# Optimization experiments

Hardware: AMD Instinct MI355X
Metric: run time of the kernel (lower is better)

## Reference

```python
import jax
import jax.numpy as jnp
from jax import lax
import numpy as np

# module hyperparameters (match init_kwargs)
IN_C, OUT_C = 32, 64
K, STRIDE, PAD, DIL = 3, 1, 1, 1
GRID_SIZE, ORDER = 5, 3
GRID_LO, GRID_HI = -1.0, 1.0
SCALE_SPLINE = 1.0
EPS = 1e-8


def _knot_grid():
    # grid = arange(-order, grid_size+order+1) * h + lo ; length = grid_size + 2*order + 1 = 12
    h = (GRID_HI - GRID_LO) / GRID_SIZE
    return jnp.arange(-ORDER, GRID_SIZE + ORDER + 1, dtype=jnp.float32) * h + GRID_LO


def _bspline_bases(x):
    """Cox-de Boor recursion. x: (N, P) -> bases: (N, P, GRID_SIZE+ORDER)."""
    grid = _knot_grid()
    xe = x[..., None]  # (N, P, 1)
    bases = ((xe >= grid[:-1]) & (xe < grid[1:])).astype(x.dtype)  # (N, P, 11)
    for k in range(1, ORDER + 1):
        left_den = jnp.maximum(grid[k:-1] - grid[:-(k + 1)], EPS)
        right_den = jnp.maximum(grid[k + 1:] - grid[1:-k], EPS)
        bases = ((xe - grid[:-(k + 1)]) / left_den * bases[..., :-1]
                 + (grid[k + 1:] - xe) / right_den * bases[..., 1:])
    return bases  # (N, P, 8)


def setup_inputs() -> dict:
    key = jax.random.key(0)
    k1, k2, k3 = jax.random.split(key, 3)
    x = jax.random.normal(k1, (4, IN_C, 56, 56), dtype=jnp.float32)
    base_weight = jax.random.normal(k2, (OUT_C, IN_C, K, K), dtype=jnp.float32) * 0.05
    spline_weight = jax.random.normal(k3, (OUT_C, IN_C * K * K, GRID_SIZE + ORDER), dtype=jnp.float32) * 0.05
    spline_scaler = jnp.ones((OUT_C,), dtype=jnp.float32)
    return {"x": x, "base_weight": base_weight,
            "spline_weight": spline_weight, "spline_scaler": spline_scaler}


def reference(x, base_weight, spline_weight, spline_scaler):
    B, C, H, W = x.shape
    pad = [(PAD, PAD), (PAD, PAD)]
    # base path: conv2d -> SiLU
    base_conv = lax.conv_general_dilated(
        x, base_weight, window_strides=(STRIDE, STRIDE), padding=pad,
        rhs_dilation=(DIL, DIL), dimension_numbers=("NCHW", "OIHW", "NCHW"))
    base_out = jax.nn.silu(base_conv)

    # unfold: (B, C*K*K, oh, ow) with torch Unfold channel ordering (c, kh, kw)
    patches = lax.conv_general_dilated_patches(
        x, filter_shape=(K, K), window_strides=(STRIDE, STRIDE), padding=pad,
        rhs_dilation=(DIL, DIL))
    oh, ow = patches.shape[2], patches.shape[3]
    num_patches = oh * ow
    # (B*num_patches, C*K*K)
    pf = patches.reshape(B, C * K * K, num_patches).transpose(0, 2, 1).reshape(-1, C * K * K)

    bases = _bspline_bases(pf)  # (N, P, F)
    # contract patch-dim and basis-dim against spline weights
    spl = jnp.einsum("npf,opf->no", bases, spline_weight) * spline_scaler  # (N, O)
    spl = spl.reshape(B, num_patches, OUT_C).transpose(0, 2, 1).reshape(B, OUT_C, oh, ow)
    return base_out + SCALE_SPLINE * spl
```

## Files before the change

### kernel.cpp

```cpp
#include <hip/hip_runtime.h>
#include <math.h>


typedef __attribute__((ext_vector_type(8)))  short bf16x8;
typedef __attribute__((ext_vector_type(4)))  float f32x4;
typedef __attribute__((ext_vector_type(16))) float f32x16;

#define MFMA32(a, b, c) __builtin_amdgcn_mfma_f32_32x32x16_bf16((a), (b), (c), 0, 0, 0)

__device__ __forceinline__ unsigned short f2bf(float f) {
    unsigned u = __builtin_bit_cast(unsigned, f);
    u = (u + 0x7fffu + ((u >> 16) & 1u)) >> 16;
    return (unsigned short)u;
}

__device__ __forceinline__ void eval_bases(float v, float bs[8]) {
    #pragma unroll
    for (int i = 0; i < 8; ++i) bs[i] = 0.0f;
    float t = (v + 2.2f) * 2.5f;
    if (t >= 0.0f && t < 11.0f) {
        int j = (int)t;
        if (j > 10) j = 10;
        float knot = (float)(j - 3) * 0.4f - 1.0f;
        float u  = (v - knot) * 2.5f;
        float um = 1.0f - u;
        float u2 = u * u, u3 = u2 * u;
        const float s6 = 1.0f / 6.0f;
        float w0 = um * um * um * s6;
        float w1 = (3.0f * u3 - 6.0f * u2 + 4.0f) * s6;
        float w2 = (-3.0f * u3 + 3.0f * u2 + 3.0f * u + 1.0f) * s6;
        float w3 = u3 * s6;
        int i0 = j - 3;
        if (i0 >= 0)               bs[i0]     = w0;
        if (i0 + 1 >= 0 && i0 < 7) bs[i0 + 1] = w1;
        if (i0 + 2 >= 0 && i0 < 6) bs[i0 + 2] = w2;
        if (i0 + 3 <= 7)           bs[i0 + 3] = w3;
    }
}

__global__ __launch_bounds__(256)
void cvt_swz_kernel(const float* __restrict__ ws, const float* __restrict__ wb,
                    unsigned short* __restrict__ wst, unsigned short* __restrict__ wbt) {
    int i = blockIdx.x * 256 + threadIdx.x;
    if (i < 147456) {
        int j = i & 7, l = (i >> 3) & 63, t = i >> 9;
        int s = t % 144, nf = t / 144;
        int oc = nf * 32 + (l & 31);
        int k  = s * 16 + (l >> 5) * 8 + j;
        wst[i] = f2bf(ws[oc * 2304 + k]);
    } else {
        int i2 = i - 147456;
        if (i2 < 18432) {
            int j = i2 & 7, l = (i2 >> 3) & 63, t = i2 >> 9;
            int s = t % 18, nf = t / 18;
            int oc = nf * 32 + (l & 31);
            int k  = s * 16 + (l >> 5) * 8 + j;
            wbt[i2] = f2bf(wb[oc * 288 + k]);
        }
    }
}

__global__ __launch_bounds__(256, 3)
void kan_mfma_kernel(const float* __restrict__ x,
                     const float* __restrict__ sc,
                     const unsigned short* __restrict__ wst,
                     const unsigned short* __restrict__ wbt,
                     float* __restrict__ out) {
    __shared__ unsigned short smem[24832];
    unsigned short* sb    = smem;
    unsigned short* patch = smem + 15360;

    const int tid = threadIdx.x;
    const int bx  = blockIdx.x;
    const int b   = bx / 98;
    const int r   = bx - b * 98;
    const int ty  = r / 7;
    const int tx  = r - ty * 7;
    const int h0  = ty * 4, w0 = tx * 8;

    const int lane = tid & 63;
    const int wv   = tid >> 6;
    const int nf   = wv & 1;
    const int kh2  = wv >> 1;
    const int m    = lane & 31;
    const int kg   = lane >> 5;
    const int py0  = m >> 3, px0 = m & 7;

    const unsigned short* bp  = wst + ((nf * 144 + kh2 * 72) * 64 + lane) * 8;
    const unsigned short* bbp = wbt + ((nf * 18  + kh2 * 9 ) * 64 + lane) * 8;

    int aoff[9];
    #pragma unroll
    for (int u = 0; u < 9; ++u) {
        int t2  = 2 * u + kg;
        int dc  = t2 / 9;
        int tap = t2 - dc * 9;
        int kh  = tap / 3;
        int kw  = tap - kh * 3;
        aoff[u] = (dc * 60 + (py0 + kh) * 10 + (px0 + kw)) * 8;
    }

    bf16x8 bufA[9], bufB[9];
    #pragma unroll
    for (int u = 0; u < 9; ++u)
        bufA[u] = *reinterpret_cast<const bf16x8*>(bp + u * 512);

    float vv[8];
    #pragma unroll
    for (int j = 0; j < 8; ++j) {
        int i = tid + j * 256;
        float val = 0.0f;
        if (i < 1920) {
            int c  = i / 60;
            int hp = i - c * 60;
            int hy = hp / 10;
            int hx = hp - hy * 10;
            int hh = h0 + hy - 1, ww = w0 + hx - 1;
            if ((unsigned)hh < 56u && (unsigned)ww < 56u)
                val = x[((b * 32 + c) * 56 + hh) * 56 + ww];
        }
        vv[j] = val;
    }
    #pragma unroll
    for (int j = 0; j < 8; ++j) {
        int i = tid + j * 256;
        if (i < 1920) {
            int c  = i / 60;
            int hp = i - c * 60;
            int hy = hp / 10;
            int hx = hp - hy * 10;
            float bs[8];
            eval_bases(vv[j], bs);
            bf16x8 pk;
            #pragma unroll
            for (int j2 = 0; j2 < 8; ++j2) pk[j2] = (short)f2bf(bs[j2]);
            *reinterpret_cast<bf16x8*>(&sb[i * 8]) = pk;
            unsigned short xb = f2bf(vv[j]);
            #pragma unroll
            for (int kh = 0; kh < 3; ++kh) {
                int py = hy - kh;
                if ((unsigned)py < 4u) {
                    #pragma unroll
                    for (int kw = 0; kw < 3; ++kw) {
                        int px = hx - kw;
                        if ((unsigned)px < 8u)
                            patch[(py * 8 + px) * 296 + c * 9 + kh * 3 + kw] = xb;
                    }
                }
            }
        }
    }
    __syncthreads();

    f32x16 acc0, acc1, accB;
    #pragma unroll
    for (int i = 0; i < 16; ++i) { acc0[i] = 0.f; acc1[i] = 0.f; accB[i] = 0.f; }

    int cbase = kh2 * 7680;
    for (int g = 0; g < 8; g += 2) {
        #pragma unroll
        for (int u = 0; u < 9; ++u)
            bufB[u] = *reinterpret_cast<const bf16x8*>(bp + ((g + 1) * 9 + u) * 512);
        #pragma unroll
        for (int u = 0; u < 9; ++u) {
            bf16x8 a = *reinterpret_cast<const bf16x8*>(&sb[cbase + aoff[u]]);
            if (u & 1) acc1 = MFMA32(a, bufA[u], acc1);
            else       acc0 = MFMA32(a, bufA[u], acc0);
        }
        cbase += 960;
        if (g + 2 < 8) {
            #pragma unroll
            for (int u = 0; u < 9; ++u)
                bufA[u] = *reinterpret_cast<const bf16x8*>(bp + ((g + 2) * 9 + u) * 512);
        }
        #pragma unroll
        for (int u = 0; u < 9; ++u) {
            bf16x8 a = *reinterpret_cast<const bf16x8*>(&sb[cbase + aoff[u]]);
            if (u & 1) acc1 = MFMA32(a, bufB[u], acc1);
            else       acc0 = MFMA32(a, bufB[u], acc0);
        }
        cbase += 960;
    }

    {
        #pragma unroll
        for (int s = 0; s < 9; ++s)
            bufA[s] = *reinterpret_cast<const bf16x8*>(bbp + s * 512);
        const unsigned short* ap = &patch[m * 296 + kh2 * 144 + kg * 8];
        #pragma unroll
        for (int s = 0; s < 9; ++s) {
            bf16x8 a = *reinterpret_cast<const bf16x8*>(ap + s * 16);
            accB = MFMA32(a, bufA[s], accB);
        }
    }

    #pragma unroll
    for (int i = 0; i < 16; ++i) acc0[i] += acc1[i];

    __syncthreads();
    float* red = (float*)smem;
    if (kh2 == 1) {
        float* dst = red + (nf * 64 + lane) * 36;
        #pragma unroll
        for (int rq = 0; rq < 4; ++rq) {
            f32x4 vS, vB;
            #pragma unroll
            for (int rr = 0; rr < 4; ++rr) { vS[rr] = acc0[rq*4+rr]; vB[rr] = accB[rq*4+rr]; }
            *reinterpret_cast<f32x4*>(dst + rq * 4)      = vS;
            *reinterpret_cast<f32x4*>(dst + 16 + rq * 4) = vB;
        }
    }
    __syncthreads();

    if (kh2 == 0) {
        const float* src = red + (nf * 64 + lane) * 36;
        #pragma unroll
        for (int rq = 0; rq < 4; ++rq) {
            f32x4 vS = *reinterpret_cast<const f32x4*>(src + rq * 4);
            f32x4 vB = *reinterpret_cast<const f32x4*>(src + 16 + rq * 4);
            #pragma unroll
            for (int rr = 0; rr < 4; ++rr) { acc0[rq*4+rr] += vS[rr]; accB[rq*4+rr] += vB[rr]; }
        }
        const int col = lane & 31;
        const int oc  = nf * 32 + col;
        const float scv = sc[oc];
        float* ob = out + ((b * 64 + oc) * 56 + h0) * 56 + w0 + 4 * kg;
        #pragma unroll
        for (int rq = 0; rq < 4; ++rq) {
            f32x4 res;
            #pragma unroll
            for (int rr = 0; rr < 4; ++rr) {
                float bv = accB[rq * 4 + rr];
                float si = bv / (1.0f + __expf(-bv));
                res[rr] = si + scv * acc0[rq * 4 + rr];
            }
            *reinterpret_cast<f32x4*>(ob + rq * 56) = res;
        }
    }
}

extern "C" void kernel_launch(void* const* d_in, const int* in_sizes, int n_in,
                              void* d_out, int out_size, void* d_ws, size_t ws_size,
                              hipStream_t stream) {
    const float* x  = (const float*)d_in[0];
    const float* wb = (const float*)d_in[1];
    const float* ws = (const float*)d_in[2];
    const float* sc = (const float*)d_in[3];
    float* out = (float*)d_out;

    unsigned short* wst = (unsigned short*)d_ws;
    unsigned short* wbt = wst + 147456;

    cvt_swz_kernel<<<648, 256, 0, stream>>>(ws, wb, wst, wbt);
    kan_mfma_kernel<<<392, 256, 0, stream>>>(x, sc, wst, wbt, out);
}
```

Measured before the change: 78.40 us.

## Fuse weight bf16 conversion into main MFMA kernel, drop preprocessing launch

Removes the separate weight conversion/swizzle kernel and has the main kernel load fp32 spline and base weights directly from global memory, converting them to bf16 in registers with a perm-based pack before each MFMA. This eliminates one kernel launch and the extra global write/read of the converted weights. In exchange, every one of the 392 blocks re-reads and re-converts the fp32 weights, which doubles the weight bytes fetched per block. The explicit double-buffered prefetch and the dual accumulators are also dropped, which may expose load latency. The conversion now rounds half-up instead of round-to-nearest-even.

```diff
diff --git a/kernel.cpp b/kernel.cpp
--- a/kernel.cpp
+++ b/kernel.cpp
@@ -12,6 +12,23 @@
     unsigned u = __builtin_bit_cast(unsigned, f);
     u = (u + 0x7fffu + ((u >> 16) & 1u)) >> 16;
     return (unsigned short)u;
+}
+
+__device__ __forceinline__ bf16x8 pack8(float4 a, float4 b) {
+    unsigned x0 = __builtin_bit_cast(unsigned, a.x) + 0x8000u;
+    unsigned x1 = __builtin_bit_cast(unsigned, a.y) + 0x8000u;
+    unsigned x2 = __builtin_bit_cast(unsigned, a.z) + 0x8000u;
+    unsigned x3 = __builtin_bit_cast(unsigned, a.w) + 0x8000u;
+    unsigned x4 = __builtin_bit_cast(unsigned, b.x) + 0x8000u;
+    unsigned x5 = __builtin_bit_cast(unsigned, b.y) + 0x8000u;
+    unsigned x6 = __builtin_bit_cast(unsigned, b.z) + 0x8000u;
+    unsigned x7 = __builtin_bit_cast(unsigned, b.w) + 0x8000u;
+    union { unsigned i[4]; bf16x8 v; } r;
+    r.i[0] = __builtin_amdgcn_perm(x1, x0, 0x07060302u);
+    r.i[1] = __builtin_amdgcn_perm(x3, x2, 0x07060302u);
+    r.i[2] = __builtin_amdgcn_perm(x5, x4, 0x07060302u);
+    r.i[3] = __builtin_amdgcn_perm(x7, x6, 0x07060302u);
+    return r.v;
 }
 
 __device__ __forceinline__ void eval_bases(float v, float bs[8]) {
@@ -38,34 +55,12 @@
     }
 }
 
-__global__ __launch_bounds__(256)
-void cvt_swz_kernel(const float* __restrict__ ws, const float* __restrict__ wb,
-                    unsigned short* __restrict__ wst, unsigned short* __restrict__ wbt) {
-    int i = blockIdx.x * 256 + threadIdx.x;
-    if (i < 147456) {
-        int j = i & 7, l = (i >> 3) & 63, t = i >> 9;
-        int s = t % 144, nf = t / 144;
-        int oc = nf * 32 + (l & 31);
-        int k  = s * 16 + (l >> 5) * 8 + j;
-        wst[i] = f2bf(ws[oc * 2304 + k]);
-    } else {
-        int i2 = i - 147456;
-        if (i2 < 18432) {
-            int j = i2 & 7, l = (i2 >> 3) & 63, t = i2 >> 9;
-            int s = t % 18, nf = t / 18;
-            int oc = nf * 32 + (l & 31);
-            int k  = s * 16 + (l >> 5) * 8 + j;
-            wbt[i2] = f2bf(wb[oc * 288 + k]);
-        }
-    }
-}
-
 __global__ __launch_bounds__(256, 3)
-void kan_mfma_kernel(const float* __restrict__ x,
-                     const float* __restrict__ sc,
-                     const unsigned short* __restrict__ wst,
-                     const unsigned short* __restrict__ wbt,
-                     float* __restrict__ out) {
+void kan_fused_kernel(const float* __restrict__ x,
+                      const float* __restrict__ wb,
+                      const float* __restrict__ ws,
+                      const float* __restrict__ sc,
+                      float* __restrict__ out) {
     __shared__ unsigned short smem[24832];
     unsigned short* sb    = smem;
     unsigned short* patch = smem + 15360;
@@ -85,9 +80,10 @@
     const int m    = lane & 31;
     const int kg   = lane >> 5;
     const int py0  = m >> 3, px0 = m & 7;
-
-    const unsigned short* bp  = wst + ((nf * 144 + kh2 * 72) * 64 + lane) * 8;
-    const unsigned short* bbp = wbt + ((nf * 18  + kh2 * 9 ) * 64 + lane) * 8;
+    const int ocl  = nf * 32 + m;
+
+    const float* bp32  = ws + ocl * 2304 + kh2 * 1152 + kg * 8;
+    const float* wbp32 = wb + ocl * 288  + kh2 * 144  + kg * 8;
 
     int aoff[9];
     #pragma unroll
@@ -99,11 +95,6 @@
         int kw  = tap - kh * 3;
         aoff[u] = (dc * 60 + (py0 + kh) * 10 + (px0 + kw)) * 8;
     }
-
-    bf16x8 bufA[9], bufB[9];
-    #pragma unroll
-    for (int u = 0; u < 9; ++u)
-        bufA[u] = *reinterpret_cast<const bf16x8*>(bp + u * 512);
 
     float vv[8];
     #pragma unroll
@@ -152,50 +143,34 @@
     }
     __syncthreads();
 
-    f32x16 acc0, acc1, accB;
-    #pragma unroll
-    for (int i = 0; i < 16; ++i) { acc0[i] = 0.f; acc1[i] = 0.f; accB[i] = 0.f; }
+    f32x16 acc, accB;
+    #pragma unroll
+    for (int i = 0; i < 16; ++i) { acc[i] = 0.f; accB[i] = 0.f; }
 
     int cbase = kh2 * 7680;
-    for (int g = 0; g < 8; g += 2) {
-        #pragma unroll
-        for (int u = 0; u < 9; ++u)
-            bufB[u] = *reinterpret_cast<const bf16x8*>(bp + ((g + 1) * 9 + u) * 512);
+    for (int g = 0; g < 8; ++g) {
         #pragma unroll
         for (int u = 0; u < 9; ++u) {
+            const float* p = bp32 + (g * 9 + u) * 16;
+            float4 f0 = *reinterpret_cast<const float4*>(p);
+            float4 f1 = *reinterpret_cast<const float4*>(p + 4);
             bf16x8 a = *reinterpret_cast<const bf16x8*>(&sb[cbase + aoff[u]]);
-            if (u & 1) acc1 = MFMA32(a, bufA[u], acc1);
-            else       acc0 = MFMA32(a, bufA[u], acc0);
+            acc = MFMA32(a, pack8(f0, f1), acc);
         }
         cbase += 960;
-        if (g + 2 < 8) {
-            #pragma unroll
-            for (int u = 0; u < 9; ++u)
-                bufA[u] = *reinterpret_cast<const bf16x8*>(bp + ((g + 2) * 9 + u) * 512);
-        }
-        #pragma unroll
-        for (int u = 0; u < 9; ++u) {
-            bf16x8 a = *reinterpret_cast<const bf16x8*>(&sb[cbase + aoff[u]]);
-            if (u & 1) acc1 = MFMA32(a, bufB[u], acc1);
-            else       acc0 = MFMA32(a, bufB[u], acc0);
-        }
-        cbase += 960;
     }
 
     {
-        #pragma unroll
-        for (int s = 0; s < 9; ++s)
-            bufA[s] = *reinterpret_cast<const bf16x8*>(bbp + s * 512);
         const unsigned short* ap = &patch[m * 296 + kh2 * 144 + kg * 8];
         #pragma unroll
         for (int s = 0; s < 9; ++s) {
+            const float* p = wbp32 + s * 16;
+            float4 f0 = *reinterpret_cast<const float4*>(p);
+            float4 f1 = *reinterpret_cast<const float4*>(p + 4);
             bf16x8 a = *reinterpret_cast<const bf16x8*>(ap + s * 16);
-            accB = MFMA32(a, bufA[s], accB);
-        }
-    }
-
-    #pragma unroll
-    for (int i = 0; i < 16; ++i) acc0[i] += acc1[i];
+            accB = MFMA32(a, pack8(f0, f1), accB);
+        }
+    }
 
     __syncthreads();
     float* red = (float*)smem;
@@ -205,7 +180,7 @@
         for (int rq = 0; rq < 4; ++rq) {
             f32x4 vS, vB;
             #pragma unroll
-            for (int rr = 0; rr < 4; ++rr) { vS[rr] = acc0[rq*4+rr]; vB[rr] = accB[rq*4+rr]; }
+            for (int rr = 0; rr < 4; ++rr) { vS[rr] = acc[rq*4+rr]; vB[rr] = accB[rq*4+rr]; }
             *reinterpret_cast<f32x4*>(dst + rq * 4)      = vS;
             *reinterpret_cast<f32x4*>(dst + 16 + rq * 4) = vB;
         }
@@ -219,10 +194,9 @@
             f32x4 vS = *reinterpret_cast<const f32x4*>(src + rq * 4);
             f32x4 vB = *reinterpret_cast<const f32x4*>(src + 16 + rq * 4);
             #pragma unroll
-            for (int rr = 0; rr < 4; ++rr) { acc0[rq*4+rr] += vS[rr]; accB[rq*4+rr] += vB[rr]; }
-        }
-        const int col = lane & 31;
-        const int oc  = nf * 32 + col;
+            for (int rr = 0; rr < 4; ++rr) { acc[rq*4+rr] += vS[rr]; accB[rq*4+rr] += vB[rr]; }
+        }
+        const int oc  = nf * 32 + m;
         const float scv = sc[oc];
         float* ob = out + ((b * 64 + oc) * 56 + h0) * 56 + w0 + 4 * kg;
         #pragma unroll
@@ -232,7 +206,7 @@
             for (int rr = 0; rr < 4; ++rr) {
                 float bv = accB[rq * 4 + rr];
                 float si = bv / (1.0f + __expf(-bv));
-                res[rr] = si + scv * acc0[rq * 4 + rr];
+                res[rr] = si + scv * acc[rq * 4 + rr];
             }
             *reinterpret_cast<f32x4*>(ob + rq * 56) = res;
         }
@@ -248,9 +222,5 @@
     const float* sc = (const float*)d_in[3];
     float* out = (float*)d_out;
 
-    unsigned short* wst = (unsigned short*)d_ws;
-    unsigned short* wbt = wst + 147456;
-
-    cvt_swz_kernel<<<648, 256, 0, stream>>>(ws, wb, wst, wbt);
-    kan_mfma_kernel<<<392, 256, 0, stream>>>(x, sc, wst, wbt, out);
-}
+    kan_fused_kernel<<<392, 256, 0, stream>>>(x, wb, ws, sc, out);
+}
```

New measurement: 104.4 us. +33.1%, slower.
